# Performance work log

Measured on AMD Instinct MI355X. Metric: run time of the kernel, lower is better.

Reference implementation:

```python
import jax, jax.numpy as jnp
import numpy as np

SEQ_LEN = 16384
HID = 2048


def setup_inputs() -> dict:
    key = jax.random.key(0)
    k1, k2, k3 = jax.random.split(key, 3)
    hidden = jax.random.normal(k1, (1, HID), dtype=jnp.float32)
    encoder_outputs = jax.random.normal(k2, (SEQ_LEN, HID), dtype=jnp.float32)
    # nn.Linear default init ~ U(-1/sqrt(H), 1/sqrt(H)); scale for realism
    W = jax.random.normal(k3, (HID, HID), dtype=jnp.float32) / np.sqrt(HID)
    b = jnp.zeros((HID,), dtype=jnp.float32)
    return {"hidden": hidden, "encoder_outputs": encoder_outputs, "W": W, "b": b}


def reference(hidden, encoder_outputs, W, b):
    # energy_i = Linear(encoder_outputs[i]) = enc @ W^T + b   -> [S, H]
    # attn_energies[i] = hidden . energy_i                   -> [S]
    energy = jnp.einsum('sh,dh->sd', encoder_outputs, W) + b      # [S, H]
    attn_energies = jnp.einsum('sd,d->s', energy, hidden[0])      # [S]
    attn = jax.nn.softmax(attn_energies, axis=0)                  # softmax over seq
    return attn[None, None, :]                                    # [1, 1, S]
```

## Files before the change

### kernel.cpp

```cpp
#include <hip/hip_runtime.h>
#include <math.h>

#define HID 2048
#define SEQ 16384

typedef float f32x4 __attribute__((ext_vector_type(4)));

__device__ __forceinline__ unsigned enc_f32(float f) {
    unsigned u = __float_as_uint(f);
    return (u & 0x80000000u) ? ~u : (u | 0x80000000u);
}
__device__ __forceinline__ float dec_f32(unsigned e) {
    unsigned u = (e & 0x80000000u) ? (e ^ 0x80000000u) : ~e;
    return __uint_as_float(u);
}

__global__ __launch_bounds__(256) void compute_v_kernel(
    const float* __restrict__ hidden,
    const float* __restrict__ W,
    float* __restrict__ v)
{
    const int h  = blockIdx.x * 256 + threadIdx.x;
    const int d0 = blockIdx.y * 32;
    float partial = 0.0f;
#pragma unroll
    for (int i = 0; i < 32; ++i) {
        const int d = d0 + i;
        partial = fmaf(hidden[d],
                       __builtin_nontemporal_load(&W[(size_t)d * HID + h]),
                       partial);
    }
    atomicAdd(&v[h], partial);
}

#define ROWS_PER_WAVE 4

__global__ __launch_bounds__(256) void compute_energies_kernel(
    const float* __restrict__ enc,
    const float* __restrict__ v,
    float* __restrict__ energies,
    unsigned* __restrict__ gmax_u)
{
    __shared__ float sred[4];

    const int lane = threadIdx.x & 63;
    const int wave = threadIdx.x >> 6;
    const int row0 = blockIdx.x * (4 * ROWS_PER_WAVE) + wave * ROWS_PER_WAVE;

    const f32x4* __restrict__ v4 = (const f32x4*)v;

    f32x4 vr[8];
#pragma unroll
    for (int j = 0; j < 8; ++j)
        vr[j] = v4[j * 64 + lane];

    float wmax = -INFINITY;
#pragma unroll
    for (int r = 0; r < ROWS_PER_WAVE; ++r) {
        const int s = row0 + r;
        const f32x4* __restrict__ row = (const f32x4*)(enc + (size_t)s * HID);

        float acc = 0.0f;
#pragma unroll
        for (int j = 0; j < 8; ++j) {
            const f32x4 a = __builtin_nontemporal_load(&row[j * 64 + lane]);
            acc = fmaf(a.x, vr[j].x, acc);
            acc = fmaf(a.y, vr[j].y, acc);
            acc = fmaf(a.z, vr[j].z, acc);
            acc = fmaf(a.w, vr[j].w, acc);
        }
#pragma unroll
        for (int off = 32; off > 0; off >>= 1)
            acc += __shfl_down(acc, off, 64);

        if (lane == 0) {
            energies[s] = acc;
            wmax = fmaxf(wmax, acc);
        }
    }

    if (lane == 0) sred[wave] = wmax;
    __syncthreads();
    if (threadIdx.x == 0) {
        const float bmax = fmaxf(fmaxf(sred[0], sred[1]), fmaxf(sred[2], sred[3]));
        atomicMax(gmax_u, enc_f32(bmax));
    }
}

__global__ __launch_bounds__(1024) void softmax_kernel(
    const float* __restrict__ energies,
    const unsigned* __restrict__ gmax_u,
    float* __restrict__ out)
{
    __shared__ float red[16];
    __shared__ float bcast;

    const int tid  = threadIdx.x;
    const int lane = tid & 63;
    const int wave = tid >> 6;

    const float4* __restrict__ e4 = (const float4*)energies;
    float4*       __restrict__ o4 = (float4*)out;

    const float gmax = dec_f32(*gmax_u);

    float vals[16];
    float lsum = 0.0f;
#pragma unroll
    for (int i = 0; i < 4; ++i) {
        const float4 a = e4[i * 1024 + tid];
        vals[i * 4 + 0] = __expf(a.x - gmax);
        vals[i * 4 + 1] = __expf(a.y - gmax);
        vals[i * 4 + 2] = __expf(a.z - gmax);
        vals[i * 4 + 3] = __expf(a.w - gmax);
        lsum += vals[i * 4 + 0] + vals[i * 4 + 1] + vals[i * 4 + 2] + vals[i * 4 + 3];
    }

#pragma unroll
    for (int off = 32; off > 0; off >>= 1)
        lsum += __shfl_down(lsum, off, 64);
    if (lane == 0) red[wave] = lsum;
    __syncthreads();
    if (tid == 0) {
        float tot = red[0];
#pragma unroll
        for (int i = 1; i < 16; ++i) tot += red[i];
        bcast = 1.0f / tot;
    }
    __syncthreads();
    const float inv = bcast;

#pragma unroll
    for (int i = 0; i < 4; ++i) {
        float4 o;
        o.x = vals[i * 4 + 0] * inv;
        o.y = vals[i * 4 + 1] * inv;
        o.z = vals[i * 4 + 2] * inv;
        o.w = vals[i * 4 + 3] * inv;
        o4[i * 1024 + tid] = o;
    }
}

extern "C" void kernel_launch(void* const* d_in, const int* in_sizes, int n_in,
                              void* d_out, int out_size, void* d_ws, size_t ws_size,
                              hipStream_t stream)
{
    const float* hidden = (const float*)d_in[0];
    const float* enc    = (const float*)d_in[1];
    const float* W      = (const float*)d_in[2];

    float* out      = (float*)d_out;
    float*    v      = (float*)d_ws;
    unsigned* gmax_u = (unsigned*)(v + HID);
    float*    energies = v + HID + 4;

    compute_v_kernel<<<dim3(HID / 256, 64), 256, 0, stream>>>(hidden, W, v);
    compute_energies_kernel<<<SEQ / (4 * ROWS_PER_WAVE), 256, 0, stream>>>(enc, v, energies, gmax_u);
    softmax_kernel<<<1, 1024, 0, stream>>>(energies, gmax_u, out);
}
```

Baseline: 205.3 us.

## Split single-block softmax into multi-block exp-sum and normalize kernels

Replaces the one-block 1024-thread softmax with two grid-wide kernels. The first computes exponentials, writes them out, and atomically accumulates a global sum. The second rescales the output by the inverse sum. This spreads the softmax across many CUs instead of one, at the cost of an extra kernel launch, extra global traffic and a float atomic. gsum is never visibly zeroed in this code.

New measurement: 206.0 us. About the same (+0.3%).

```diff
diff --git a/kernel.cpp b/kernel.cpp
--- a/kernel.cpp
+++ b/kernel.cpp
@@ -87,58 +87,40 @@
     }
 }
 
-__global__ __launch_bounds__(1024) void softmax_kernel(
+__global__ __launch_bounds__(64) void exp_sum_kernel(
     const float* __restrict__ energies,
     const unsigned* __restrict__ gmax_u,
+    float* __restrict__ gsum,
     float* __restrict__ out)
 {
-    __shared__ float red[16];
-    __shared__ float bcast;
-
-    const int tid  = threadIdx.x;
-    const int lane = tid & 63;
-    const int wave = tid >> 6;
-
-    const float4* __restrict__ e4 = (const float4*)energies;
-    float4*       __restrict__ o4 = (float4*)out;
-
+    const int idx  = blockIdx.x * 64 + threadIdx.x;
     const float gmax = dec_f32(*gmax_u);
 
-    float vals[16];
-    float lsum = 0.0f;
-#pragma unroll
-    for (int i = 0; i < 4; ++i) {
-        const float4 a = e4[i * 1024 + tid];
-        vals[i * 4 + 0] = __expf(a.x - gmax);
-        vals[i * 4 + 1] = __expf(a.y - gmax);
-        vals[i * 4 + 2] = __expf(a.z - gmax);
-        vals[i * 4 + 3] = __expf(a.w - gmax);
-        lsum += vals[i * 4 + 0] + vals[i * 4 + 1] + vals[i * 4 + 2] + vals[i * 4 + 3];
-    }
+    const f32x4 a = ((const f32x4*)energies)[idx];
+    f32x4 ex;
+    ex.x = __expf(a.x - gmax);
+    ex.y = __expf(a.y - gmax);
+    ex.z = __expf(a.z - gmax);
+    ex.w = __expf(a.w - gmax);
+    ((f32x4*)out)[idx] = ex;
 
+    float sum = ex.x + ex.y + ex.z + ex.w;
 #pragma unroll
     for (int off = 32; off > 0; off >>= 1)
-        lsum += __shfl_down(lsum, off, 64);
-    if (lane == 0) red[wave] = lsum;
-    __syncthreads();
-    if (tid == 0) {
-        float tot = red[0];
-#pragma unroll
-        for (int i = 1; i < 16; ++i) tot += red[i];
-        bcast = 1.0f / tot;
-    }
-    __syncthreads();
-    const float inv = bcast;
+        sum += __shfl_down(sum, off, 64);
+    if (threadIdx.x == 0)
+        atomicAdd(gsum, sum);
+}
 
-#pragma unroll
-    for (int i = 0; i < 4; ++i) {
-        float4 o;
-        o.x = vals[i * 4 + 0] * inv;
-        o.y = vals[i * 4 + 1] * inv;
-        o.z = vals[i * 4 + 2] * inv;
-        o.w = vals[i * 4 + 3] * inv;
-        o4[i * 1024 + tid] = o;
-    }
+__global__ __launch_bounds__(64) void normalize_kernel(
+    const float* __restrict__ gsum,
+    float* __restrict__ out)
+{
+    const int idx = blockIdx.x * 64 + threadIdx.x;
+    const float inv = 1.0f / *gsum;
+    f32x4 o = ((f32x4*)out)[idx];
+    o.x *= inv; o.y *= inv; o.z *= inv; o.w *= inv;
+    ((f32x4*)out)[idx] = o;
 }
 
 extern "C" void kernel_launch(void* const* d_in, const int* in_sizes, int n_in,
@@ -152,9 +134,11 @@
     float* out      = (float*)d_out;
     float*    v      = (float*)d_ws;
     unsigned* gmax_u = (unsigned*)(v + HID);
+    float*    gsum   = (float*)(gmax_u + 1);
     float*    energies = v + HID + 4;
 
     compute_v_kernel<<<dim3(HID / 256, 64), 256, 0, stream>>>(hidden, W, v);
     compute_energies_kernel<<<SEQ / (4 * ROWS_PER_WAVE), 256, 0, stream>>>(enc, v, energies, gmax_u);
-    softmax_kernel<<<1, 1024, 0, stream>>>(energies, gmax_u, out);
+    exp_sum_kernel<<<SEQ / 256, 64, 0, stream>>>(energies, gmax_u, gsum, out);
+    normalize_kernel<<<SEQ / 256, 64, 0, stream>>>(gsum, out);
 }
```
